# Kernel tuning notes

Measured on AMD Instinct MI355X. Metric: run time of the kernel, lower is better.

The kernel has to match this reference:

```python
import jax, jax.numpy as jnp
import numpy as np

B, A, N_IN = 128, 96, 128  # molecules, atoms per molecule, feature dim
H1, H2 = 64, 1             # gated-equivariant MLP widths: 128 -> 64 -> 1


def _mlp(x, W1, b1, W2, b2):
    return jax.nn.silu(x @ W1 + b1) @ W2 + b2


def _gated_block(s, v, Wmix, Ws1, bs1, Ws2, bs2, n_out, sact):
    # s: [N, n_sin], v: [N, 3, n_vin]
    vmix = jnp.einsum('ndi,io->ndo', v, Wmix)          # [N, 3, 2*n_out]
    vV, vW = vmix[..., :n_out], vmix[..., n_out:]
    vVn = jnp.linalg.norm(vV, axis=-2)                 # [N, n_out]
    x = _mlp(jnp.concatenate([s, vVn], axis=-1), Ws1, bs1, Ws2, bs2)
    s_out, gate = x[..., :n_out], x[..., n_out:]
    v_out = gate[:, None, :] * vW                      # [N, 3, n_out]
    if sact:
        s_out = jax.nn.silu(s_out)
    return s_out, v_out


def setup_inputs():
    key = jax.random.key(0)
    ks = iter(jax.random.split(key, 40))
    def W(shape):
        return jax.random.normal(next(ks), shape, jnp.float32) / np.sqrt(shape[0]).astype(np.float32)
    N = B * A
    return dict(
        positions=jax.random.normal(next(ks), (N, 3), jnp.float32) * 3.0,
        scalar_rep=jax.random.normal(next(ks), (N, N_IN), jnp.float32),
        vector_rep=jax.random.normal(next(ks), (N, 3, N_IN), jnp.float32),
        mix_W1=W((N_IN, 2 * H1)),
        sc1_W1=W((N_IN + H1, N_IN)), sc1_b1=jnp.zeros((N_IN,), jnp.float32),
        sc1_W2=W((N_IN, 2 * H1)), sc1_b2=jnp.zeros((2 * H1,), jnp.float32),
        mix_W2=W((H1, 2 * H2)),
        sc2_W1=W((H1 + H2, H1)), sc2_b1=jnp.zeros((H1,), jnp.float32),
        sc2_W2=W((H1, 2 * H2)), sc2_b2=jnp.zeros((2 * H2,), jnp.float32),
        vv_W1=W((9, 30)), vv_b1=jnp.zeros((30,), jnp.float32), vv_W2=W((30, 9)), vv_b2=jnp.zeros((9,), jnp.float32),
        vr_W1=W((9, 30)), vr_b1=jnp.zeros((30,), jnp.float32), vr_W2=W((30, 9)), vr_b2=jnp.zeros((9,), jnp.float32),
        s_W1=W((2, 30)), s_b1=jnp.zeros((30,), jnp.float32), s_W2=W((30, 9)), s_b2=jnp.zeros((9,), jnp.float32),
        h_W1=W((9, 30)), h_b1=jnp.zeros((30,), jnp.float32), h_W2=W((30, 9)), h_b2=jnp.zeros((9,), jnp.float32),
        n_atoms=jnp.full((B,), A, dtype=jnp.int32),
    )


def reference(positions, scalar_rep, vector_rep,
              mix_W1, sc1_W1, sc1_b1, sc1_W2, sc1_b2,
              mix_W2, sc2_W1, sc2_b1, sc2_W2, sc2_b2,
              vv_W1, vv_b1, vv_W2, vv_b2,
              vr_W1, vr_b1, vr_W2, vr_b2,
              s_W1, s_b1, s_W2, s_b2,
              h_W1, h_b1, h_W2, h_b2, n_atoms):
    # outnet: gated equivariant MLP 128 -> 64 (silu on scalars) -> 1 (no sact)
    s, v = _gated_block(scalar_rep, vector_rep, mix_W1, sc1_W1, sc1_b1, sc1_W2, sc1_b2, H1, True)
    s, v = _gated_block(s, v, mix_W2, sc2_W1, sc2_b1, sc2_W2, sc2_b2, H2, False)
    l0 = s[:, 0].reshape(B, A)          # [B, A]
    l1 = v[:, :, 0].reshape(B, A, 3)    # [B, A, 3]
    pos = positions.reshape(B, A, 3)
    # per-pair outer products, flattened 3x3 -> 9 (row-major k,l as in torch view)
    vv = jnp.einsum('bik,bjl->bijkl', l1, l1).reshape(B, A, A, 9)
    vr = jnp.einsum('bik,bjl->bijkl', l1, pos).reshape(B, A, A, 9)
    vv = _mlp(vv, vv_W1, vv_b1, vv_W2, vv_b2)
    vr = _mlp(vr, vr_W1, vr_b1, vr_W2, vr_b2)
    sp = jnp.stack([jnp.broadcast_to(l0[:, :, None], (B, A, A)),
                    jnp.broadcast_to(l0[:, None, :], (B, A, A))], axis=-1)  # [B,A,A,2] = (s_i, s_j)
    sp = _mlp(sp, s_W1, s_b1, s_W2, s_b2)
    h = _mlp(vv + vr + sp, h_W1, h_b1, h_W2, h_b2).reshape(B, A, A, 3, 3)
    # permute(0,2,1,3) per molecule -> block Hessian [3A, 3A]
    h = jnp.transpose(h, (0, 1, 3, 2, 4)).reshape(B, 3 * A, 3 * A)
    return h.reshape(-1, 27)
```

## Files before the change

kernel.cpp:

```cpp
#include <hip/hip_runtime.h>
#include <cstddef>

#define A_ATOMS 96
#define BATCH   128
#define NNODES  12288
#define NROWS3  36864

__device__ __forceinline__ float silu_f(float x) {
    float e = __expf(-x);
    return x * __builtin_amdgcn_rcpf(1.0f + e);
}

__global__ __launch_bounds__(256)
void gemm96_k(const float* __restrict__ A, const float* __restrict__ W,
              const float* __restrict__ srep,
              float* __restrict__ vmix, float* __restrict__ xin) {
    __shared__ float smem[96 * 128];
    float* As = smem;
    float* Bs = smem + 768;
    const int t  = threadIdx.x;
    const int tx = t & 15;
    const int ty = t >> 4;
    const int row0 = blockIdx.x * 96;

    float acc[6][8];
#pragma unroll
    for (int i = 0; i < 6; i++)
#pragma unroll
        for (int j = 0; j < 8; j++) acc[i][j] = 0.0f;

    for (int kc = 0; kc < 128; kc += 8) {
        if (t < 192) {
            const int m  = t >> 1;
            const int k4 = (t & 1) * 4;
            float4 av = *(const float4*)(A + (size_t)(row0 + m) * 128 + kc + k4);
            As[(k4 + 0) * 96 + m] = av.x; As[(k4 + 1) * 96 + m] = av.y;
            As[(k4 + 2) * 96 + m] = av.z; As[(k4 + 3) * 96 + m] = av.w;
        }
        {
            const int kb = t >> 5;
            const int n4 = (t & 31) * 4;
            *(float4*)&Bs[kb * 128 + n4] = *(const float4*)(W + (size_t)(kc + kb) * 128 + n4);
        }
        __syncthreads();
#pragma unroll
        for (int k = 0; k < 8; k++) {
            float bf[8], af[6];
            *(float4*)&bf[0] = *(const float4*)&Bs[k * 128 + tx * 8];
            *(float4*)&bf[4] = *(const float4*)&Bs[k * 128 + tx * 8 + 4];
            *(float2*)&af[0] = *(const float2*)&As[k * 96 + ty * 6];
            *(float2*)&af[2] = *(const float2*)&As[k * 96 + ty * 6 + 2];
            *(float2*)&af[4] = *(const float2*)&As[k * 96 + ty * 6 + 4];
#pragma unroll
            for (int i = 0; i < 6; i++)
#pragma unroll
                for (int j = 0; j < 8; j++) acc[i][j] += af[i] * bf[j];
        }
        __syncthreads();
    }

    float* Cs = smem;
#pragma unroll
    for (int i = 0; i < 6; i++) {
        const int m = ty * 6 + i;
        float* gp = vmix + (size_t)(row0 + m) * 128 + tx * 8;
        *(float4*)gp       = *(float4*)&acc[i][0];
        *(float4*)(gp + 4) = *(float4*)&acc[i][4];
        *(float4*)&Cs[m * 128 + tx * 8]     = *(float4*)&acc[i][0];
        *(float4*)&Cs[m * 128 + tx * 8 + 4] = *(float4*)&acc[i][4];
    }
    __syncthreads();

    const int node0 = row0 / 3;
#pragma unroll
    for (int it = 0; it < 4; it++) {
        const int idx = it * 256 + t;
        const int a   = idx >> 5;
        const int c4  = (idx & 31) * 4;
        *(float4*)(xin + (size_t)(node0 + a) * 192 + c4) =
            *(const float4*)(srep + (size_t)(node0 + a) * 128 + c4);
    }
#pragma unroll
    for (int it = 0; it < 8; it++) {
        const int idx = it * 256 + t;
        const int a   = idx >> 6;
        const int c   = idx & 63;
        const float v0 = Cs[(3 * a + 0) * 128 + c];
        const float v1 = Cs[(3 * a + 1) * 128 + c];
        const float v2 = Cs[(3 * a + 2) * 128 + c];
        xin[(size_t)(node0 + a) * 192 + 128 + c] = sqrtf(v0 * v0 + v1 * v1 + v2 * v2);
    }
}

template<int ACT>
__global__ __launch_bounds__(256)
void gemmN_k(const float* __restrict__ A, const float* __restrict__ W,
             const float* __restrict__ bias, float* __restrict__ C,
             int M, int K) {
    __shared__ float As[8][64];
    __shared__ float Bs[8][64];
    const int t  = threadIdx.x;
    const int tx = t & 15;
    const int ty = t >> 4;
    const int row0 = blockIdx.x * 64;
    const int col0 = blockIdx.y * 64;

    float acc[4][4];
#pragma unroll
    for (int i = 0; i < 4; i++)
#pragma unroll
        for (int j = 0; j < 4; j++) acc[i][j] = 0.0f;

    for (int kc = 0; kc < K; kc += 8) {
        {
            const int m  = t >> 2;
            const int k2 = (t & 3) * 2;
            float2 av = *(const float2*)(A + (size_t)(row0 + m) * K + kc + k2);
            As[k2 + 0][m] = av.x; As[k2 + 1][m] = av.y;
        }
        {
            const int kb = t >> 5;
            const int n2 = (t & 31) * 2;
            *(float2*)&Bs[kb][n2] = *(const float2*)(W + (size_t)(kc + kb) * 128 + col0 + n2);
        }
        __syncthreads();
#pragma unroll
        for (int k = 0; k < 8; k++) {
            float af[4], bf[4];
            *(float4*)&af[0] = *(const float4*)&As[k][ty * 4];
            *(float4*)&bf[0] = *(const float4*)&Bs[k][tx * 4];
#pragma unroll
            for (int i = 0; i < 4; i++)
#pragma unroll
                for (int j = 0; j < 4; j++) acc[i][j] += af[i] * bf[j];
        }
        __syncthreads();
    }
#pragma unroll
    for (int i = 0; i < 4; i++) {
        const int row = row0 + ty * 4 + i;
        float v[4];
#pragma unroll
        for (int j = 0; j < 4; j++) {
            float x = acc[i][j] + bias[col0 + tx * 4 + j];
            if (ACT == 1) x = silu_f(x);
            v[j] = x;
        }
        *(float4*)(C + (size_t)row * 128 + col0 + tx * 4) = *(float4*)&v[0];
    }
}

#define RED64(v) { v += __shfl_xor(v, 1); v += __shfl_xor(v, 2); v += __shfl_xor(v, 4); \
                   v += __shfl_xor(v, 8); v += __shfl_xor(v, 16); v += __shfl_xor(v, 32); }

__global__ __launch_bounds__(256)
void glue2_k(const float* __restrict__ x1, const float* __restrict__ vmix,
             const float* __restrict__ mixW2,
             const float* __restrict__ W1, const float* __restrict__ b1,
             const float* __restrict__ W2, const float* __restrict__ b2,
             float* __restrict__ l0v, float* __restrict__ l1v) {
    __shared__ float s1s[4][64];
    const int t = threadIdx.x;
    const int w = t >> 6, lane = t & 63;
    const int n = blockIdx.x * 4 + w;

    const float xa = x1[(size_t)n * 128 + lane];
    const float xb = x1[(size_t)n * 128 + 64 + lane];
    const float s1 = silu_f(xa);
    const float v1_0 = xb * vmix[((size_t)(3 * n + 0)) * 128 + 64 + lane];
    const float v1_1 = xb * vmix[((size_t)(3 * n + 1)) * 128 + 64 + lane];
    const float v1_2 = xb * vmix[((size_t)(3 * n + 2)) * 128 + 64 + lane];

    const float w0 = mixW2[lane * 2 + 0], w1 = mixW2[lane * 2 + 1];
    float p0 = v1_0 * w0, p1 = v1_0 * w1;
    float p2 = v1_1 * w0, p3 = v1_1 * w1;
    float p4 = v1_2 * w0, p5 = v1_2 * w1;
    RED64(p0); RED64(p1); RED64(p2); RED64(p3); RED64(p4); RED64(p5);
    const float vn2 = sqrtf(p0 * p0 + p2 * p2 + p4 * p4);

    s1s[w][lane] = s1;
    __syncthreads();

    float acc = b1[lane] + vn2 * W1[64 * 64 + lane];
#pragma unroll 8
    for (int i2 = 0; i2 < 64; i2++) acc += s1s[w][i2] * W1[i2 * 64 + lane];
    const float h2 = silu_f(acc);

    float q0 = h2 * W2[lane * 2 + 0];
    float q1 = h2 * W2[lane * 2 + 1];
    RED64(q0); RED64(q1);

    if (lane == 0) {
        const float s_out = q0 + b2[0];
        const float gate  = q1 + b2[1];
        l0v[n] = s_out;
        l1v[(size_t)n * 3 + 0] = gate * p1;
        l1v[(size_t)n * 3 + 1] = gate * p3;
        l1v[(size_t)n * 3 + 2] = gate * p5;
    }
}

__global__ __launch_bounds__(256)
void pairpre_k(const float* __restrict__ l1v, const float* __restrict__ pos,
               const float* __restrict__ l0v,
               const float* __restrict__ vvW1, const float* __restrict__ vrW1,
               const float* __restrict__ sW1, const float* __restrict__ sb1,
               float* __restrict__ Pv, float* __restrict__ Pr,
               float* __restrict__ Ps) {
    const int h = threadIdx.x;
    const int j = blockIdx.x * 8 + threadIdx.y;
    if (h >= 30) return;
    const float lj0 = l1v[j * 3 + 0], lj1 = l1v[j * 3 + 1], lj2 = l1v[j * 3 + 2];
    const float pj0 = pos[j * 3 + 0], pj1 = pos[j * 3 + 1], pj2 = pos[j * 3 + 2];
#pragma unroll
    for (int a = 0; a < 3; a++) {
        float v = lj0 * vvW1[(3 * a + 0) * 30 + h] + lj1 * vvW1[(3 * a + 1) * 30 + h]
                + lj2 * vvW1[(3 * a + 2) * 30 + h];
        float r = pj0 * vrW1[(3 * a + 0) * 30 + h] + pj1 * vrW1[(3 * a + 1) * 30 + h]
                + pj2 * vrW1[(3 * a + 2) * 30 + h];
        Pv[(size_t)(a * 30 + h) * NNODES + j] = v;
        Pr[(size_t)(a * 30 + h) * NNODES + j] = r;
    }
    Ps[(size_t)h * NNODES + j] = sb1[h] + l0v[j] * sW1[30 + h];
}

__global__ __launch_bounds__(192)
void pair_k(const float* __restrict__ l0v, const float* __restrict__ l1v,
            const float* __restrict__ Pv, const float* __restrict__ Pr,
            const float* __restrict__ Ps,
            const float* __restrict__ vvb1, const float* __restrict__ vrb1,
            const float* __restrict__ sW1,
            const float* __restrict__ vvW2, const float* __restrict__ vrW2,
            const float* __restrict__ sW2,
            const float* __restrict__ vvb2, const float* __restrict__ vrb2,
            const float* __restrict__ sb2,
            const float* __restrict__ hW1,  const float* __restrict__ hb1,
            const float* __restrict__ hW2,  const float* __restrict__ hb2,
            float* __restrict__ out) {
    const int t = threadIdx.x;
    const int b = blockIdx.y;
    const int di = (t >= 96) ? 1 : 0;
    const int i = blockIdx.x * 2 + di;
    const int j = t - di * 96;
    const int ni = b * A_ATOMS + i;
    const int nj = b * A_ATOMS + j;

    const float li0 = l1v[ni * 3 + 0], li1 = l1v[ni * 3 + 1], li2 = l1v[ni * 3 + 2];
    const float s0i = l0v[ni];

    float t9[9];
#pragma unroll
    for (int l = 0; l < 9; l++) t9[l] = vvb2[l] + vrb2[l] + sb2[l];

    for (int h = 0; h < 30; h++) {
        float av = vvb1[h] + li0 * Pv[(size_t)h * NNODES + nj]
                           + li1 * Pv[(size_t)(30 + h) * NNODES + nj]
                           + li2 * Pv[(size_t)(60 + h) * NNODES + nj];
        float ar = vrb1[h] + li0 * Pr[(size_t)h * NNODES + nj]
                           + li1 * Pr[(size_t)(30 + h) * NNODES + nj]
                           + li2 * Pr[(size_t)(60 + h) * NNODES + nj];
        float as = Ps[(size_t)h * NNODES + nj] + s0i * sW1[h];
        av = silu_f(av); ar = silu_f(ar); as = silu_f(as);
#pragma unroll
        for (int l = 0; l < 9; l++)
            t9[l] += av * vvW2[h * 9 + l] + ar * vrW2[h * 9 + l] + as * sW2[h * 9 + l];
    }

    float o9[9];
#pragma unroll
    for (int l = 0; l < 9; l++) o9[l] = hb2[l];
    for (int h = 0; h < 30; h++) {
        float a = hb1[h];
#pragma unroll
        for (int m = 0; m < 9; m++) a += t9[m] * hW1[m * 30 + h];
        a = silu_f(a);
#pragma unroll
        for (int l = 0; l < 9; l++) o9[l] += a * hW2[h * 9 + l];
    }

    const size_t rb = (size_t)(b * A_ATOMS + i);
#pragma unroll
    for (int k = 0; k < 3; k++) {
        const size_t off = (rb * 3 + k) * 288 + (size_t)j * 3;
        out[off + 0] = o9[3 * k + 0];
        out[off + 1] = o9[3 * k + 1];
        out[off + 2] = o9[3 * k + 2];
    }
}

extern "C" void kernel_launch(void* const* d_in, const int* in_sizes, int n_in,
                              void* d_out, int out_size, void* d_ws, size_t ws_size,
                              hipStream_t stream) {
    const float* pos   = (const float*)d_in[0];
    const float* srep  = (const float*)d_in[1];
    const float* vrep  = (const float*)d_in[2];
    const float* mixW1 = (const float*)d_in[3];
    const float* sc1W1 = (const float*)d_in[4];
    const float* sc1b1 = (const float*)d_in[5];
    const float* sc1W2 = (const float*)d_in[6];
    const float* sc1b2 = (const float*)d_in[7];
    const float* mixW2 = (const float*)d_in[8];
    const float* sc2W1 = (const float*)d_in[9];
    const float* sc2b1 = (const float*)d_in[10];
    const float* sc2W2 = (const float*)d_in[11];
    const float* sc2b2 = (const float*)d_in[12];
    const float* vvW1  = (const float*)d_in[13];
    const float* vvb1  = (const float*)d_in[14];
    const float* vvW2  = (const float*)d_in[15];
    const float* vvb2  = (const float*)d_in[16];
    const float* vrW1  = (const float*)d_in[17];
    const float* vrb1  = (const float*)d_in[18];
    const float* vrW2  = (const float*)d_in[19];
    const float* vrb2  = (const float*)d_in[20];
    const float* sW1   = (const float*)d_in[21];
    const float* sb1   = (const float*)d_in[22];
    const float* sW2   = (const float*)d_in[23];
    const float* sb2   = (const float*)d_in[24];
    const float* hW1   = (const float*)d_in[25];
    const float* hb1   = (const float*)d_in[26];
    const float* hW2   = (const float*)d_in[27];
    const float* hb2   = (const float*)d_in[28];

    float* ws   = (float*)d_ws;
    float* vmix = ws;
    float* xin  = vmix + 4718592;
    float* hmid = xin  + 2359296;
    float* x1   = hmid + 1572864;
    float* l0v  = x1   + 1572864;
    float* l1v  = l0v  + 12288;
    float* Pv   = ws;
    float* Pr   = Pv + 1105920;
    float* Ps   = Pr + 1105920;
    float* outf = (float*)d_out;

    gemm96_k<<<NROWS3 / 96, 256, 0, stream>>>(vrep, mixW1, srep, vmix, xin);
    gemmN_k<1><<<dim3(NNODES / 64, 2), 256, 0, stream>>>(xin, sc1W1, sc1b1, hmid, NNODES, 192);
    gemmN_k<0><<<dim3(NNODES / 64, 2), 256, 0, stream>>>(hmid, sc1W2, sc1b2, x1, NNODES, 128);
    glue2_k<<<NNODES / 4, 256, 0, stream>>>(x1, vmix, mixW2, sc2W1, sc2b1, sc2W2, sc2b2,
                                            l0v, l1v);
    pairpre_k<<<NNODES / 8, dim3(32, 8), 0, stream>>>(l1v, pos, l0v, vvW1, vrW1,
                                                      sW1, sb1, Pv, Pr, Ps);
    pair_k<<<dim3(A_ATOMS / 2, BATCH), 192, 0, stream>>>(
        l0v, l1v, Pv, Pr, Ps,
        vvb1, vrb1, sW1,
        vvW2, vrW2, sW2,
        vvb2, vrb2, sb2,
        hW1, hb1, hW2, hb2,
        outf);
}
```

Measured before the change: 306.0 us.

## Fuse node-level GEMMs, gating and pair precompute into a single kernel

Replaces the separate vector-mix GEMM, two scalar MLP GEMMs, second gated block and pair-precompute kernels with one node_k kernel. Each block handles 16 nodes and keeps vmix, the MLP input, hidden activations and outputs in shared memory. This removes the global-memory round trips of the large intermediates and several kernel launches. In exchange, every block reloads the full weight matrices and runs small 16-row GEMM tiles. Each block also uses a large shared-memory footprint, which may limit occupancy.

New measurement: 324.6 us. 6.1% more time.

```diff
diff --git a/kernel.cpp b/kernel.cpp
--- a/kernel.cpp
+++ b/kernel.cpp
@@ -4,224 +4,243 @@
 #define A_ATOMS 96
 #define BATCH   128
 #define NNODES  12288
-#define NROWS3  36864
+#define NB      16
+#define XS      196
+#define WS      132
 
 __device__ __forceinline__ float silu_f(float x) {
     float e = __expf(-x);
     return x * __builtin_amdgcn_rcpf(1.0f + e);
 }
 
+#define RED64(v) { v += __shfl_xor(v, 1); v += __shfl_xor(v, 2); v += __shfl_xor(v, 4); \
+                   v += __shfl_xor(v, 8); v += __shfl_xor(v, 16); v += __shfl_xor(v, 32); }
+
 __global__ __launch_bounds__(256)
-void gemm96_k(const float* __restrict__ A, const float* __restrict__ W,
-              const float* __restrict__ srep,
-              float* __restrict__ vmix, float* __restrict__ xin) {
-    __shared__ float smem[96 * 128];
-    float* As = smem;
-    float* Bs = smem + 768;
+void node_k(const float* __restrict__ vrep, const float* __restrict__ mixW1,
+            const float* __restrict__ srep,
+            const float* __restrict__ sc1W1, const float* __restrict__ sc1b1,
+            const float* __restrict__ sc1W2, const float* __restrict__ sc1b2,
+            const float* __restrict__ mixW2,
+            const float* __restrict__ sc2W1, const float* __restrict__ sc2b1,
+            const float* __restrict__ sc2W2, const float* __restrict__ sc2b2,
+            const float* __restrict__ pos,
+            const float* __restrict__ vvW1, const float* __restrict__ vrW1,
+            const float* __restrict__ sW1, const float* __restrict__ sb1,
+            float* __restrict__ l0v, float* __restrict__ l1v,
+            float* __restrict__ Pv, float* __restrict__ Pr,
+            float* __restrict__ Ps) {
+    __shared__ float As[8 * 48];
+    __shared__ float Bt[8 * 128];
+    __shared__ float Cs[48 * WS];
+    __shared__ float xinS[NB * XS];
+    __shared__ float workS[NB * WS];
+    __shared__ float s1s[4][64];
+    __shared__ float l0s[NB];
+    __shared__ float l1s[NB * 3];
+
     const int t  = threadIdx.x;
     const int tx = t & 15;
     const int ty = t >> 4;
-    const int row0 = blockIdx.x * 96;
-
-    float acc[6][8];
-#pragma unroll
-    for (int i = 0; i < 6; i++)
-#pragma unroll
-        for (int j = 0; j < 8; j++) acc[i][j] = 0.0f;
-
-    for (int kc = 0; kc < 128; kc += 8) {
-        if (t < 192) {
-            const int m  = t >> 1;
-            const int k4 = (t & 1) * 4;
-            float4 av = *(const float4*)(A + (size_t)(row0 + m) * 128 + kc + k4);
-            As[(k4 + 0) * 96 + m] = av.x; As[(k4 + 1) * 96 + m] = av.y;
-            As[(k4 + 2) * 96 + m] = av.z; As[(k4 + 3) * 96 + m] = av.w;
-        }
-        {
-            const int kb = t >> 5;
-            const int n4 = (t & 31) * 4;
-            *(float4*)&Bs[kb * 128 + n4] = *(const float4*)(W + (size_t)(kc + kb) * 128 + n4);
-        }
-        __syncthreads();
-#pragma unroll
-        for (int k = 0; k < 8; k++) {
-            float bf[8], af[6];
-            *(float4*)&bf[0] = *(const float4*)&Bs[k * 128 + tx * 8];
-            *(float4*)&bf[4] = *(const float4*)&Bs[k * 128 + tx * 8 + 4];
-            *(float2*)&af[0] = *(const float2*)&As[k * 96 + ty * 6];
-            *(float2*)&af[2] = *(const float2*)&As[k * 96 + ty * 6 + 2];
-            *(float2*)&af[4] = *(const float2*)&As[k * 96 + ty * 6 + 4];
-#pragma unroll
-            for (int i = 0; i < 6; i++)
-#pragma unroll
-                for (int j = 0; j < 8; j++) acc[i][j] += af[i] * bf[j];
-        }
-        __syncthreads();
-    }
-
-    float* Cs = smem;
-#pragma unroll
-    for (int i = 0; i < 6; i++) {
-        const int m = ty * 6 + i;
-        float* gp = vmix + (size_t)(row0 + m) * 128 + tx * 8;
-        *(float4*)gp       = *(float4*)&acc[i][0];
-        *(float4*)(gp + 4) = *(float4*)&acc[i][4];
-        *(float4*)&Cs[m * 128 + tx * 8]     = *(float4*)&acc[i][0];
-        *(float4*)&Cs[m * 128 + tx * 8 + 4] = *(float4*)&acc[i][4];
-    }
-    __syncthreads();
-
-    const int node0 = row0 / 3;
-#pragma unroll
-    for (int it = 0; it < 4; it++) {
+    const int row0  = blockIdx.x * 48;
+    const int node0 = blockIdx.x * NB;
+
+    {
+        float acc[3][8];
+#pragma unroll
+        for (int i = 0; i < 3; i++)
+#pragma unroll
+            for (int j = 0; j < 8; j++) acc[i][j] = 0.0f;
+
+        for (int kc = 0; kc < 128; kc += 8) {
+            if (t < 96) {
+                const int m  = t >> 1;
+                const int k4 = (t & 1) * 4;
+                float4 av = *(const float4*)(vrep + (size_t)(row0 + m) * 128 + kc + k4);
+                As[(k4 + 0) * 48 + m] = av.x; As[(k4 + 1) * 48 + m] = av.y;
+                As[(k4 + 2) * 48 + m] = av.z; As[(k4 + 3) * 48 + m] = av.w;
+            }
+            {
+                const int kb = t >> 5;
+                const int n4 = (t & 31) * 4;
+                *(float4*)&Bt[kb * 128 + n4] = *(const float4*)(mixW1 + (size_t)(kc + kb) * 128 + n4);
+            }
+            __syncthreads();
+#pragma unroll
+            for (int k = 0; k < 8; k++) {
+                float bf[8], af[3];
+                *(float4*)&bf[0] = *(const float4*)&Bt[k * 128 + tx * 8];
+                *(float4*)&bf[4] = *(const float4*)&Bt[k * 128 + tx * 8 + 4];
+                af[0] = As[k * 48 + ty * 3 + 0];
+                af[1] = As[k * 48 + ty * 3 + 1];
+                af[2] = As[k * 48 + ty * 3 + 2];
+#pragma unroll
+                for (int i = 0; i < 3; i++)
+#pragma unroll
+                    for (int j = 0; j < 8; j++) acc[i][j] += af[i] * bf[j];
+            }
+            __syncthreads();
+        }
+#pragma unroll
+        for (int i = 0; i < 3; i++) {
+            const int m = ty * 3 + i;
+            *(float4*)&Cs[m * WS + tx * 8]     = *(float4*)&acc[i][0];
+            *(float4*)&Cs[m * WS + tx * 8 + 4] = *(float4*)&acc[i][4];
+        }
+    }
+    __syncthreads();
+
+#pragma unroll
+    for (int it = 0; it < 2; it++) {
         const int idx = it * 256 + t;
         const int a   = idx >> 5;
         const int c4  = (idx & 31) * 4;
-        *(float4*)(xin + (size_t)(node0 + a) * 192 + c4) =
+        *(float4*)&xinS[a * XS + c4] =
             *(const float4*)(srep + (size_t)(node0 + a) * 128 + c4);
     }
 #pragma unroll
-    for (int it = 0; it < 8; it++) {
+    for (int it = 0; it < 4; it++) {
         const int idx = it * 256 + t;
         const int a   = idx >> 6;
         const int c   = idx & 63;
-        const float v0 = Cs[(3 * a + 0) * 128 + c];
-        const float v1 = Cs[(3 * a + 1) * 128 + c];
-        const float v2 = Cs[(3 * a + 2) * 128 + c];
-        xin[(size_t)(node0 + a) * 192 + 128 + c] = sqrtf(v0 * v0 + v1 * v1 + v2 * v2);
-    }
-}
-
-template<int ACT>
-__global__ __launch_bounds__(256)
-void gemmN_k(const float* __restrict__ A, const float* __restrict__ W,
-             const float* __restrict__ bias, float* __restrict__ C,
-             int M, int K) {
-    __shared__ float As[8][64];
-    __shared__ float Bs[8][64];
-    const int t  = threadIdx.x;
-    const int tx = t & 15;
-    const int ty = t >> 4;
-    const int row0 = blockIdx.x * 64;
-    const int col0 = blockIdx.y * 64;
-
-    float acc[4][4];
-#pragma unroll
-    for (int i = 0; i < 4; i++)
-#pragma unroll
-        for (int j = 0; j < 4; j++) acc[i][j] = 0.0f;
-
-    for (int kc = 0; kc < K; kc += 8) {
-        {
-            const int m  = t >> 2;
-            const int k2 = (t & 3) * 2;
-            float2 av = *(const float2*)(A + (size_t)(row0 + m) * K + kc + k2);
-            As[k2 + 0][m] = av.x; As[k2 + 1][m] = av.y;
-        }
-        {
-            const int kb = t >> 5;
-            const int n2 = (t & 31) * 2;
-            *(float2*)&Bs[kb][n2] = *(const float2*)(W + (size_t)(kc + kb) * 128 + col0 + n2);
-        }
-        __syncthreads();
-#pragma unroll
-        for (int k = 0; k < 8; k++) {
-            float af[4], bf[4];
-            *(float4*)&af[0] = *(const float4*)&As[k][ty * 4];
-            *(float4*)&bf[0] = *(const float4*)&Bs[k][tx * 4];
-#pragma unroll
-            for (int i = 0; i < 4; i++)
-#pragma unroll
-                for (int j = 0; j < 4; j++) acc[i][j] += af[i] * bf[j];
-        }
-        __syncthreads();
-    }
-#pragma unroll
-    for (int i = 0; i < 4; i++) {
-        const int row = row0 + ty * 4 + i;
-        float v[4];
-#pragma unroll
-        for (int j = 0; j < 4; j++) {
-            float x = acc[i][j] + bias[col0 + tx * 4 + j];
-            if (ACT == 1) x = silu_f(x);
-            v[j] = x;
-        }
-        *(float4*)(C + (size_t)row * 128 + col0 + tx * 4) = *(float4*)&v[0];
-    }
-}
-
-#define RED64(v) { v += __shfl_xor(v, 1); v += __shfl_xor(v, 2); v += __shfl_xor(v, 4); \
-                   v += __shfl_xor(v, 8); v += __shfl_xor(v, 16); v += __shfl_xor(v, 32); }
-
-__global__ __launch_bounds__(256)
-void glue2_k(const float* __restrict__ x1, const float* __restrict__ vmix,
-             const float* __restrict__ mixW2,
-             const float* __restrict__ W1, const float* __restrict__ b1,
-             const float* __restrict__ W2, const float* __restrict__ b2,
-             float* __restrict__ l0v, float* __restrict__ l1v) {
-    __shared__ float s1s[4][64];
-    const int t = threadIdx.x;
-    const int w = t >> 6, lane = t & 63;
-    const int n = blockIdx.x * 4 + w;
-
-    const float xa = x1[(size_t)n * 128 + lane];
-    const float xb = x1[(size_t)n * 128 + 64 + lane];
-    const float s1 = silu_f(xa);
-    const float v1_0 = xb * vmix[((size_t)(3 * n + 0)) * 128 + 64 + lane];
-    const float v1_1 = xb * vmix[((size_t)(3 * n + 1)) * 128 + 64 + lane];
-    const float v1_2 = xb * vmix[((size_t)(3 * n + 2)) * 128 + 64 + lane];
-
-    const float w0 = mixW2[lane * 2 + 0], w1 = mixW2[lane * 2 + 1];
-    float p0 = v1_0 * w0, p1 = v1_0 * w1;
-    float p2 = v1_1 * w0, p3 = v1_1 * w1;
-    float p4 = v1_2 * w0, p5 = v1_2 * w1;
-    RED64(p0); RED64(p1); RED64(p2); RED64(p3); RED64(p4); RED64(p5);
-    const float vn2 = sqrtf(p0 * p0 + p2 * p2 + p4 * p4);
-
-    s1s[w][lane] = s1;
-    __syncthreads();
-
-    float acc = b1[lane] + vn2 * W1[64 * 64 + lane];
-#pragma unroll 8
-    for (int i2 = 0; i2 < 64; i2++) acc += s1s[w][i2] * W1[i2 * 64 + lane];
-    const float h2 = silu_f(acc);
-
-    float q0 = h2 * W2[lane * 2 + 0];
-    float q1 = h2 * W2[lane * 2 + 1];
-    RED64(q0); RED64(q1);
-
-    if (lane == 0) {
-        const float s_out = q0 + b2[0];
-        const float gate  = q1 + b2[1];
-        l0v[n] = s_out;
-        l1v[(size_t)n * 3 + 0] = gate * p1;
-        l1v[(size_t)n * 3 + 1] = gate * p3;
-        l1v[(size_t)n * 3 + 2] = gate * p5;
-    }
-}
-
-__global__ __launch_bounds__(256)
-void pairpre_k(const float* __restrict__ l1v, const float* __restrict__ pos,
-               const float* __restrict__ l0v,
-               const float* __restrict__ vvW1, const float* __restrict__ vrW1,
-               const float* __restrict__ sW1, const float* __restrict__ sb1,
-               float* __restrict__ Pv, float* __restrict__ Pr,
-               float* __restrict__ Ps) {
-    const int h = threadIdx.x;
-    const int j = blockIdx.x * 8 + threadIdx.y;
-    if (h >= 30) return;
-    const float lj0 = l1v[j * 3 + 0], lj1 = l1v[j * 3 + 1], lj2 = l1v[j * 3 + 2];
-    const float pj0 = pos[j * 3 + 0], pj1 = pos[j * 3 + 1], pj2 = pos[j * 3 + 2];
-#pragma unroll
-    for (int a = 0; a < 3; a++) {
-        float v = lj0 * vvW1[(3 * a + 0) * 30 + h] + lj1 * vvW1[(3 * a + 1) * 30 + h]
-                + lj2 * vvW1[(3 * a + 2) * 30 + h];
-        float r = pj0 * vrW1[(3 * a + 0) * 30 + h] + pj1 * vrW1[(3 * a + 1) * 30 + h]
-                + pj2 * vrW1[(3 * a + 2) * 30 + h];
-        Pv[(size_t)(a * 30 + h) * NNODES + j] = v;
-        Pr[(size_t)(a * 30 + h) * NNODES + j] = r;
-    }
-    Ps[(size_t)h * NNODES + j] = sb1[h] + l0v[j] * sW1[30 + h];
+        const float v0 = Cs[(3 * a + 0) * WS + c];
+        const float v1 = Cs[(3 * a + 1) * WS + c];
+        const float v2 = Cs[(3 * a + 2) * WS + c];
+        xinS[a * XS + 128 + c] = sqrtf(v0 * v0 + v1 * v1 + v2 * v2);
+    }
+    __syncthreads();
+
+    {
+        float acc3[8];
+#pragma unroll
+        for (int j = 0; j < 8; j++) acc3[j] = 0.0f;
+        for (int kc = 0; kc < 192; kc += 8) {
+            {
+                const int kb = t >> 5;
+                const int n4 = (t & 31) * 4;
+                *(float4*)&Bt[kb * 128 + n4] = *(const float4*)(sc1W1 + (size_t)(kc + kb) * 128 + n4);
+            }
+            __syncthreads();
+            float af[8];
+            *(float4*)&af[0] = *(const float4*)&xinS[ty * XS + kc];
+            *(float4*)&af[4] = *(const float4*)&xinS[ty * XS + kc + 4];
+#pragma unroll
+            for (int k = 0; k < 8; k++) {
+                float bf[8];
+                *(float4*)&bf[0] = *(const float4*)&Bt[k * 128 + tx * 8];
+                *(float4*)&bf[4] = *(const float4*)&Bt[k * 128 + tx * 8 + 4];
+#pragma unroll
+                for (int j = 0; j < 8; j++) acc3[j] += af[k] * bf[j];
+            }
+            __syncthreads();
+        }
+#pragma unroll
+        for (int j = 0; j < 8; j++)
+            workS[ty * WS + tx * 8 + j] = silu_f(acc3[j] + sc1b1[tx * 8 + j]);
+    }
+    __syncthreads();
+
+    {
+        float acc4[8];
+#pragma unroll
+        for (int j = 0; j < 8; j++) acc4[j] = 0.0f;
+        for (int kc = 0; kc < 128; kc += 8) {
+            {
+                const int kb = t >> 5;
+                const int n4 = (t & 31) * 4;
+                *(float4*)&Bt[kb * 128 + n4] = *(const float4*)(sc1W2 + (size_t)(kc + kb) * 128 + n4);
+            }
+            __syncthreads();
+            float af[8];
+            *(float4*)&af[0] = *(const float4*)&workS[ty * WS + kc];
+            *(float4*)&af[4] = *(const float4*)&workS[ty * WS + kc + 4];
+#pragma unroll
+            for (int k = 0; k < 8; k++) {
+                float bf[8];
+                *(float4*)&bf[0] = *(const float4*)&Bt[k * 128 + tx * 8];
+                *(float4*)&bf[4] = *(const float4*)&Bt[k * 128 + tx * 8 + 4];
+#pragma unroll
+                for (int j = 0; j < 8; j++) acc4[j] += af[k] * bf[j];
+            }
+            __syncthreads();
+        }
+#pragma unroll
+        for (int j = 0; j < 8; j++)
+            xinS[ty * WS + tx * 8 + j] = acc4[j] + sc1b2[tx * 8 + j];
+    }
+    __syncthreads();
+
+    {
+        const int w = t >> 6, lane = t & 63;
+        const float w0 = mixW2[lane * 2 + 0], w1 = mixW2[lane * 2 + 1];
+        const float wq0 = sc2W2[lane * 2 + 0], wq1 = sc2W2[lane * 2 + 1];
+        const float bb1 = sc2b1[lane];
+        const float wn  = sc2W1[64 * 64 + lane];
+#pragma unroll
+        for (int r = 0; r < 4; r++) {
+            const int nl = r * 4 + w;
+            const float xa = xinS[nl * WS + lane];
+            const float xb = xinS[nl * WS + 64 + lane];
+            const float s1 = silu_f(xa);
+            const float v1_0 = xb * Cs[(3 * nl + 0) * WS + 64 + lane];
+            const float v1_1 = xb * Cs[(3 * nl + 1) * WS + 64 + lane];
+            const float v1_2 = xb * Cs[(3 * nl + 2) * WS + 64 + lane];
+
+            float p0 = v1_0 * w0, p1 = v1_0 * w1;
+            float p2 = v1_1 * w0, p3 = v1_1 * w1;
+            float p4 = v1_2 * w0, p5 = v1_2 * w1;
+            RED64(p0); RED64(p1); RED64(p2); RED64(p3); RED64(p4); RED64(p5);
+            const float vn2 = sqrtf(p0 * p0 + p2 * p2 + p4 * p4);
+
+            s1s[w][lane] = s1;
+            __builtin_amdgcn_s_waitcnt(0);
+            float acc = bb1 + vn2 * wn;
+            for (int i2 = 0; i2 < 64; i2++) acc += s1s[w][i2] * sc2W1[i2 * 64 + lane];
+            const float h2 = silu_f(acc);
+
+            float q0 = h2 * wq0;
+            float q1 = h2 * wq1;
+            RED64(q0); RED64(q1);
+
+            if (lane == 0) {
+                const int n = node0 + nl;
+                const float s_out = q0 + sc2b2[0];
+                const float gate  = q1 + sc2b2[1];
+                l0v[n] = s_out;
+                l1v[(size_t)n * 3 + 0] = gate * p1;
+                l1v[(size_t)n * 3 + 1] = gate * p3;
+                l1v[(size_t)n * 3 + 2] = gate * p5;
+                l0s[nl] = s_out;
+                l1s[nl * 3 + 0] = gate * p1;
+                l1s[nl * 3 + 1] = gate * p3;
+                l1s[nl * 3 + 2] = gate * p5;
+            }
+        }
+    }
+    __syncthreads();
+
+    {
+        const int h = t & 31;
+        if (h < 30) {
+#pragma unroll
+            for (int half = 0; half < 2; half++) {
+                const int nl = (t >> 5) + half * 8;
+                const int j  = node0 + nl;
+                const float lj0 = l1s[nl * 3 + 0], lj1 = l1s[nl * 3 + 1], lj2 = l1s[nl * 3 + 2];
+                const float pj0 = pos[j * 3 + 0], pj1 = pos[j * 3 + 1], pj2 = pos[j * 3 + 2];
+#pragma unroll
+                for (int a = 0; a < 3; a++) {
+                    float v = lj0 * vvW1[(3 * a + 0) * 30 + h] + lj1 * vvW1[(3 * a + 1) * 30 + h]
+                            + lj2 * vvW1[(3 * a + 2) * 30 + h];
+                    float r = pj0 * vrW1[(3 * a + 0) * 30 + h] + pj1 * vrW1[(3 * a + 1) * 30 + h]
+                            + pj2 * vrW1[(3 * a + 2) * 30 + h];
+                    Pv[(size_t)(a * 30 + h) * NNODES + j] = v;
+                    Pr[(size_t)(a * 30 + h) * NNODES + j] = r;
+                }
+                Ps[(size_t)h * NNODES + j] = sb1[h] + l0s[nl] * sW1[30 + h];
+            }
+        }
+    }
 }
 
 __global__ __launch_bounds__(192)
@@ -321,25 +340,21 @@
     const float* hW2   = (const float*)d_in[27];
     const float* hb2   = (const float*)d_in[28];
 
-    float* ws   = (float*)d_ws;
-    float* vmix = ws;
-    float* xin  = vmix + 4718592;
-    float* hmid = xin  + 2359296;
-    float* x1   = hmid + 1572864;
-    float* l0v  = x1   + 1572864;
-    float* l1v  = l0v  + 12288;
-    float* Pv   = ws;
-    float* Pr   = Pv + 1105920;
-    float* Ps   = Pr + 1105920;
+    float* ws  = (float*)d_ws;
+    float* Pv  = ws;
+    float* Pr  = Pv + 1105920;
+    float* Ps  = Pr + 1105920;
+    float* l0v = Ps + 368640;
+    float* l1v = l0v + 12288;
     float* outf = (float*)d_out;
 
-    gemm96_k<<<NROWS3 / 96, 256, 0, stream>>>(vrep, mixW1, srep, vmix, xin);
-    gemmN_k<1><<<dim3(NNODES / 64, 2), 256, 0, stream>>>(xin, sc1W1, sc1b1, hmid, NNODES, 192);
-    gemmN_k<0><<<dim3(NNODES / 64, 2), 256, 0, stream>>>(hmid, sc1W2, sc1b2, x1, NNODES, 128);
-    glue2_k<<<NNODES / 4, 256, 0, stream>>>(x1, vmix, mixW2, sc2W1, sc2b1, sc2W2, sc2b2,
-                                            l0v, l1v);
-    pairpre_k<<<NNODES / 8, dim3(32, 8), 0, stream>>>(l1v, pos, l0v, vvW1, vrW1,
-                                                      sW1, sb1, Pv, Pr, Ps);
+    node_k<<<NNODES / NB, 256, 0, stream>>>(
+        vrep, mixW1, srep,
+        sc1W1, sc1b1, sc1W2, sc1b2,
+        mixW2, sc2W1, sc2b1, sc2W2, sc2b2,
+        pos, vvW1, vrW1, sW1, sb1,
+        l0v, l1v, Pv, Pr, Ps);
+
     pair_k<<<dim3(A_ATOMS / 2, BATCH), 192, 0, stream>>>(
         l0v, l1v, Pv, Pr, Ps,
         vvb1, vrb1, sW1,
```
